# Kernel optimization log

Hardware: AMD Instinct MI355X
Metric: run time of the kernel (lower is better)

Reference implementation:

```python
import jax, jax.numpy as jnp
import numpy as np

N_NODES = 100000
N_EDGES = 1600000
D_IN = 64
D_H = 64
D_LIN = 256
D_OUT = 128
N_GRAPHS = 64
BN_EPS = 1e-5


def setup_inputs() -> dict:
    key = jax.random.key(0)
    ks = jax.random.split(key, 16)

    def lin(k, fan_in, fan_out):
        # kaiming-ish init, scale 1/sqrt(fan_in)
        return jax.random.normal(k, (fan_in, fan_out), jnp.float32) / np.float32(np.sqrt(fan_in))

    inp = {}
    inp["x"] = jax.random.normal(ks[0], (N_NODES, D_IN), jnp.float32)
    inp["edge_index"] = jax.random.randint(ks[1], (2, N_EDGES), 0, N_NODES, jnp.int32)
    inp["batch"] = jnp.sort(jax.random.randint(ks[2], (N_NODES,), 0, N_GRAPHS, jnp.int32))

    dims = [(D_IN, D_H), (D_H, D_H), (D_H, D_H)]
    ki = 3
    for l, (di, do) in enumerate(dims):
        inp[f"conv{l}_w1"] = lin(ks[ki], di, do); ki += 1
        inp[f"conv{l}_b1"] = jnp.zeros((do,), jnp.float32)
        inp[f"conv{l}_w2"] = lin(ks[ki], do, do); ki += 1
        inp[f"conv{l}_b2"] = jnp.zeros((do,), jnp.float32)
    for l in range(2):
        inp[f"bn{l}_gamma"] = jnp.ones((D_H,), jnp.float32)
        inp[f"bn{l}_beta"] = jnp.zeros((D_H,), jnp.float32)
    inp["mp_w1"] = lin(ks[ki], D_H, D_LIN); ki += 1
    inp["mp_b1"] = jnp.zeros((D_LIN,), jnp.float32)
    inp["mp_w2"] = lin(ks[ki], D_LIN, D_OUT)
    inp["mp_b2"] = jnp.zeros((D_OUT,), jnp.float32)
    return inp


def gin_conv(x, src, dst, w1, b1, w2, b2):
    # GINConv with eps=0: nn((1+eps)*x + sum_{j->i} x_j)
    agg = jax.ops.segment_sum(x[src], dst, num_segments=N_NODES)  # [N, d]
    h = x + agg
    h = jnp.maximum(h @ w1 + b1, 0.0)
    return h @ w2 + b2


def batch_norm(x, gamma, beta):
    # BatchNorm1d over node dim (training-mode batch statistics)
    mean = jnp.mean(x, axis=0)
    var = jnp.var(x, axis=0)
    return (x - mean) * jax.lax.rsqrt(var + BN_EPS) * gamma + beta


def reference(x, edge_index, batch,
              conv0_w1, conv0_b1, conv0_w2, conv0_b2,
              conv1_w1, conv1_b1, conv1_w2, conv1_b2,
              conv2_w1, conv2_b1, conv2_w2, conv2_b2,
              bn0_gamma, bn0_beta, bn1_gamma, bn1_beta,
              mp_w1, mp_b1, mp_w2, mp_b2):
    src, dst = edge_index[0], edge_index[1]
    convs = [(conv0_w1, conv0_b1, conv0_w2, conv0_b2),
             (conv1_w1, conv1_b1, conv1_w2, conv1_b2),
             (conv2_w1, conv2_b1, conv2_w2, conv2_b2)]
    bns = [(bn0_gamma, bn0_beta), (bn1_gamma, bn1_beta)]

    h = x
    # first conv_num_layers-1 layers: conv -> BN -> ReLU (dropout = identity in eval)
    for i in range(2):
        w1, b1, w2, b2 = convs[i]
        h = gin_conv(h, src, dst, w1, b1, w2, b2)
        h = batch_norm(h, bns[i][0], bns[i][1])
        h = jnp.maximum(h, 0.0)
    # last conv
    w1, b1, w2, b2 = convs[2]
    h = gin_conv(h, src, dst, w1, b1, w2, b2)
    # global add pool over graphs
    pooled = jax.ops.segment_sum(h, batch, num_segments=N_GRAPHS)  # [G, d]
    emb = pooled
    out = jnp.maximum(pooled @ mp_w1 + mp_b1, 0.0)  # dropout = identity in eval
    out = out @ mp_w2 + mp_b2
    return (out, emb)
```

## Files before the change

kernel.cpp:

```cpp
#include <hip/hip_runtime.h>

#define N_NODES 100000
#define N_EDGES 1600000
#define D 64
#define N_GRAPHS 64
#define D_LIN 256
#define D_OUT 128
#define BN_EPS 1e-5f
#define NBUCK 782
#define BIN_CH 16384
#define ESTAGE 1024

typedef unsigned short ushort;
typedef unsigned int uint;
typedef float floatx4 __attribute__((ext_vector_type(4)));
typedef uint uintx2 __attribute__((ext_vector_type(2)));

__device__ __forceinline__ float4 ld4(const float* p) { return *(const float4*)p; }

__device__ __forceinline__ uint f2bf(float f) {
  uint u = __float_as_uint(f);
  return (u + 0x7FFFu + ((u >> 16) & 1u)) >> 16;
}

__global__ __launch_bounds__(256) void k_cvt(const float* __restrict__ in,
                                             ushort* __restrict__ out, int n8) {
  int i = blockIdx.x * 256 + threadIdx.x;
  if (i < n8) {
    float4 a = ((const float4*)in)[2 * i];
    float4 b = ((const float4*)in)[2 * i + 1];
    uint4 o;
    o.x = f2bf(a.x) | (f2bf(a.y) << 16);
    o.y = f2bf(a.z) | (f2bf(a.w) << 16);
    o.z = f2bf(b.x) | (f2bf(b.y) << 16);
    o.w = f2bf(b.z) | (f2bf(b.w) << 16);
    ((uint4*)out)[i] = o;
  }
}

__global__ __launch_bounds__(256) void k_hist(const int* __restrict__ dstA,
                                              int* __restrict__ bcnt) {
  __shared__ int lh[NBUCK];
  for (int i = threadIdx.x; i < NBUCK; i += 256) lh[i] = 0;
  __syncthreads();
  int i = blockIdx.x * 256 + threadIdx.x;
  const int stride = gridDim.x * 256;
  for (; i < N_EDGES; i += stride) atomicAdd(&lh[dstA[i] >> 7], 1);
  __syncthreads();
  for (int i = threadIdx.x; i < NBUCK; i += 256)
    if (lh[i]) atomicAdd(&bcnt[i], lh[i]);
}

__global__ __launch_bounds__(1024) void k_bscan(const int* __restrict__ bcnt,
                                                int* __restrict__ boff,
                                                int* __restrict__ bcur) {
  __shared__ int s[1024];
  int t = threadIdx.x;
  int v = (t < NBUCK) ? bcnt[t] : 0;
  s[t] = v;
  __syncthreads();
  for (int off = 1; off < 1024; off <<= 1) {
    int u = (t >= off) ? s[t - off] : 0;
    __syncthreads();
    s[t] += u;
    __syncthreads();
  }
  if (t < NBUCK) {
    boff[t] = s[t] - v;
    bcur[t] = s[t] - v;
  }
}

__global__ __launch_bounds__(256) void k_bin(const int* __restrict__ srcA,
                                             const int* __restrict__ dstA,
                                             int* __restrict__ bcur,
                                             uint2* __restrict__ pairs) {
  __shared__ int lh[NBUCK];
  __shared__ int lbase[NBUCK];
  const int tid = threadIdx.x;
  for (int i = tid; i < NBUCK; i += 256) lh[i] = 0;
  __syncthreads();
  const int e0 = blockIdx.x * BIN_CH;
  const int e1 = min(e0 + BIN_CH, N_EDGES);
  for (int i = e0 + tid; i < e1; i += 256) atomicAdd(&lh[dstA[i] >> 7], 1);
  __syncthreads();
  for (int b = tid; b < NBUCK; b += 256) {
    int c = lh[b];
    if (c) lbase[b] = atomicAdd(&bcur[b], c);
  }
  __syncthreads();
  for (int b = tid; b < NBUCK; b += 256) lh[b] = 0;
  __syncthreads();
  for (int i = e0 + tid; i < e1; i += 256) {
    int d = dstA[i];
    int b = d >> 7;
    int p = lbase[b] + atomicAdd(&lh[b], 1);
    pairs[p] = make_uint2((uint)srcA[i], (uint)d);
  }
}

__global__ __launch_bounds__(256) void k_bucket(const uint2* __restrict__ pairs,
                                                const int* __restrict__ boff,
                                                const int* __restrict__ bcnt,
                                                int* __restrict__ rowptr,
                                                int* __restrict__ colidx) {
  __shared__ int ldeg[128], lsc[128], lcur[128];
  __shared__ int stage[4096];
  const int tid = threadIdx.x;
  const int b = blockIdx.x;
  const int node0 = b << 7;
  const int base = boff[b], cnt = bcnt[b];
  if (tid < 128) ldeg[tid] = 0;
  __syncthreads();
  for (int i = tid; i < cnt; i += 256) atomicAdd(&ldeg[pairs[base + i].y & 127], 1);
  __syncthreads();
  if (tid < 128) lsc[tid] = ldeg[tid];
  __syncthreads();
  for (int off = 1; off < 128; off <<= 1) {
    int u = (tid < 128 && tid >= off) ? lsc[tid - off] : 0;
    __syncthreads();
    if (tid < 128) lsc[tid] += u;
    __syncthreads();
  }
  if (tid < 128) {
    int excl = lsc[tid] - ldeg[tid];
    lcur[tid] = excl;
    int node = node0 + tid;
    if (node < N_NODES) rowptr[node] = base + excl;
  }
  if (b == NBUCK - 1 && tid == 0) rowptr[N_NODES] = N_EDGES;
  __syncthreads();
  if (cnt <= 4096) {
    for (int i = tid; i < cnt; i += 256) {
      uint2 pr = pairs[base + i];
      int p = atomicAdd(&lcur[pr.y & 127], 1);
      stage[p] = (int)pr.x;
    }
    __syncthreads();
    for (int i = tid; i < cnt; i += 256) colidx[base + i] = stage[i];
  } else {
    for (int i = tid; i < cnt; i += 256) {
      uint2 pr = pairs[base + i];
      int p = atomicAdd(&lcur[pr.y & 127], 1);
      colidx[base + p] = (int)pr.x;
    }
  }
}

template <int APPLY_BN, int EMIT_STATS, int OUT_BF>
__global__ __launch_bounds__(128, 6) void k_conv(
    const ushort* __restrict__ h_in, const float* __restrict__ ss,
    const int* __restrict__ rowptr, const int* __restrict__ colidx,
    const float* __restrict__ w1, const float* __restrict__ b1,
    const float* __restrict__ w2, const float* __restrict__ b2,
    float* __restrict__ h_out_f, ushort* __restrict__ h_out_bf,
    float* __restrict__ stats) {
  __shared__ float sT[32][68];
  __shared__ float sSum[64], sSq[64];
  __shared__ int sEdge[ESTAGE];
  __shared__ int sRp[33];

  const int tid = threadIdx.x;
  const int wave = tid >> 6, lane = tid & 63;
  const int g = lane >> 3;
  const int fl = (lane & 7) << 3;
  const int row0 = blockIdx.x * 32;

  if (EMIT_STATS && tid < 64) { sSum[tid] = 0.f; sSq[tid] = 0.f; }
  if (tid < 33) sRp[tid] = rowptr[row0 + tid];
  __syncthreads();

  const int ebase = sRp[0];
  const int ecnt = sRp[32] - ebase;
  const int estage = min(ecnt, ESTAGE);
  for (int i = tid; i < estage; i += 128)
    sEdge[i] = __builtin_nontemporal_load(colidx + ebase + i);
  __syncthreads();

  float sc[8], sh[8];
  if (APPLY_BN) {
    float4 a = ld4(&ss[fl]), b = ld4(&ss[fl + 4]);
    float4 c = ld4(&ss[64 + fl]), d = ld4(&ss[64 + fl + 4]);
    sc[0] = a.x; sc[1] = a.y; sc[2] = a.z; sc[3] = a.w;
    sc[4] = b.x; sc[5] = b.y; sc[6] = b.z; sc[7] = b.w;
    sh[0] = c.x; sh[1] = c.y; sh[2] = c.z; sh[3] = c.w;
    sh[4] = d.x; sh[5] = d.y; sh[6] = d.z; sh[7] = d.w;
  }

#define ACC8(u)                                                        \
  {                                                                    \
    float f0 = __uint_as_float((u).x << 16);                           \
    float f1 = __uint_as_float((u).x & 0xffff0000u);                   \
    float f2 = __uint_as_float((u).y << 16);                           \
    float f3 = __uint_as_float((u).y & 0xffff0000u);                   \
    float f4 = __uint_as_float((u).z << 16);                           \
    float f5 = __uint_as_float((u).z & 0xffff0000u);                   \
    float f6 = __uint_as_float((u).w << 16);                           \
    float f7 = __uint_as_float((u).w & 0xffff0000u);                   \
    if (APPLY_BN) {                                                    \
      f0 = fmaxf(fmaf(f0, sc[0], sh[0]), 0.f);                         \
      f1 = fmaxf(fmaf(f1, sc[1], sh[1]), 0.f);                         \
      f2 = fmaxf(fmaf(f2, sc[2], sh[2]), 0.f);                         \
      f3 = fmaxf(fmaf(f3, sc[3], sh[3]), 0.f);                         \
      f4 = fmaxf(fmaf(f4, sc[4], sh[4]), 0.f);                         \
      f5 = fmaxf(fmaf(f5, sc[5], sh[5]), 0.f);                         \
      f6 = fmaxf(fmaf(f6, sc[6], sh[6]), 0.f);                         \
      f7 = fmaxf(fmaf(f7, sc[7], sh[7]), 0.f);                         \
    }                                                                  \
    acc[0] += f0; acc[1] += f1; acc[2] += f2; acc[3] += f3;            \
    acc[4] += f4; acc[5] += f5; acc[6] += f6; acc[7] += f7;            \
  }
#define GATHER(s) *(const uint4*)(h_in + ((size_t)(s) << 6) + fl)

#pragma unroll
  for (int b = 0; b < 2; ++b) {
    const int r = (wave << 4) + (b << 3) + g;
    const int row = row0 + r;
    float acc[8] = {0.f, 0.f, 0.f, 0.f, 0.f, 0.f, 0.f, 0.f};
    {
      uint4 u = GATHER(row);
      ACC8(u);
    }
    const int re0 = sRp[r] - ebase;
    const int re1g = sRp[r + 1] - ebase;
    const int re1 = min(re1g, estage);
    int e = re0;
    for (; e + 7 < re1; e += 8) {
      int s0 = sEdge[e];
      int s1 = sEdge[e + 1];
      int s2 = sEdge[e + 2];
      int s3 = sEdge[e + 3];
      int s4 = sEdge[e + 4];
      int s5 = sEdge[e + 5];
      int s6 = sEdge[e + 6];
      int s7 = sEdge[e + 7];
      uint4 u0 = GATHER(s0);
      uint4 u1 = GATHER(s1);
      uint4 u2 = GATHER(s2);
      uint4 u3 = GATHER(s3);
      uint4 u4 = GATHER(s4);
      uint4 u5 = GATHER(s5);
      uint4 u6 = GATHER(s6);
      uint4 u7 = GATHER(s7);
      ACC8(u0); ACC8(u1); ACC8(u2); ACC8(u3);
      ACC8(u4); ACC8(u5); ACC8(u6); ACC8(u7);
    }
    if (e < re1) {
      const int em = re1 - 1;
      int s0 = sEdge[e];
      int s1 = sEdge[min(e + 1, em)];
      int s2 = sEdge[min(e + 2, em)];
      int s3 = sEdge[min(e + 3, em)];
      int s4 = sEdge[min(e + 4, em)];
      int s5 = sEdge[min(e + 5, em)];
      int s6 = sEdge[min(e + 6, em)];
      int s7 = sEdge[min(e + 7, em)];
      uint4 u0 = GATHER(s0);
      uint4 u1 = GATHER(s1);
      uint4 u2 = GATHER(s2);
      uint4 u3 = GATHER(s3);
      uint4 u4 = GATHER(s4);
      uint4 u5 = GATHER(s5);
      uint4 u6 = GATHER(s6);
      uint4 u7 = GATHER(s7);
      ACC8(u0);
      if (e + 1 < re1) ACC8(u1);
      if (e + 2 < re1) ACC8(u2);
      if (e + 3 < re1) ACC8(u3);
      if (e + 4 < re1) ACC8(u4);
      if (e + 5 < re1) ACC8(u5);
      if (e + 6 < re1) ACC8(u6);
      if (e + 7 < re1) ACC8(u7);
    }
    for (int eg2 = ebase + max(re0, estage); eg2 < ebase + re1g; ++eg2) {
      int s0 = colidx[eg2];
      uint4 u0 = GATHER(s0);
      ACC8(u0);
    }
    *(float4*)&sT[r][fl] = make_float4(acc[0], acc[1], acc[2], acc[3]);
    *(float4*)&sT[r][fl + 4] = make_float4(acc[4], acc[5], acc[6], acc[7]);
  }
#undef GATHER
#undef ACC8
  __syncthreads();

  const int tc = tid & 15, tr = tid >> 4;

  float hreg[4][4];
  {
    float acc[4][4];
#pragma unroll
    for (int i = 0; i < 4; ++i)
#pragma unroll
      for (int j = 0; j < 4; ++j) acc[i][j] = 0.f;
#pragma unroll 8
    for (int k = 0; k < 64; ++k) {
      const float4 b = ld4(&w1[(k << 6) + (tc << 2)]);
#pragma unroll
      for (int i = 0; i < 4; ++i) {
        const float a = sT[(tr << 2) + i][k];
        acc[i][0] = fmaf(a, b.x, acc[i][0]);
        acc[i][1] = fmaf(a, b.y, acc[i][1]);
        acc[i][2] = fmaf(a, b.z, acc[i][2]);
        acc[i][3] = fmaf(a, b.w, acc[i][3]);
      }
    }
    const float4 bb = ld4(&b1[tc << 2]);
#pragma unroll
    for (int i = 0; i < 4; ++i) {
      hreg[i][0] = fmaxf(acc[i][0] + bb.x, 0.f);
      hreg[i][1] = fmaxf(acc[i][1] + bb.y, 0.f);
      hreg[i][2] = fmaxf(acc[i][2] + bb.z, 0.f);
      hreg[i][3] = fmaxf(acc[i][3] + bb.w, 0.f);
    }
  }
  __syncthreads();
#pragma unroll
  for (int i = 0; i < 4; ++i)
    *(float4*)&sT[(tr << 2) + i][tc << 2] = *(float4*)&hreg[i][0];
  __syncthreads();

  {
    float acc[4][4];
#pragma unroll
    for (int i = 0; i < 4; ++i)
#pragma unroll
      for (int j = 0; j < 4; ++j) acc[i][j] = 0.f;
#pragma unroll 8
    for (int k = 0; k < 64; ++k) {
      const float4 b = ld4(&w2[(k << 6) + (tc << 2)]);
#pragma unroll
      for (int i = 0; i < 4; ++i) {
        const float a = sT[(tr << 2) + i][k];
        acc[i][0] = fmaf(a, b.x, acc[i][0]);
        acc[i][1] = fmaf(a, b.y, acc[i][1]);
        acc[i][2] = fmaf(a, b.z, acc[i][2]);
        acc[i][3] = fmaf(a, b.w, acc[i][3]);
      }
    }
    const float4 bb = ld4(&b2[tc << 2]);
    float p[4] = {0.f, 0.f, 0.f, 0.f}, q[4] = {0.f, 0.f, 0.f, 0.f};
#pragma unroll
    for (int i = 0; i < 4; ++i) {
      const int row = row0 + (tr << 2) + i;
      float4 o;
      o.x = acc[i][0] + bb.x;
      o.y = acc[i][1] + bb.y;
      o.z = acc[i][2] + bb.z;
      o.w = acc[i][3] + bb.w;
      if (OUT_BF) {
        uintx2 o2;
        o2.x = f2bf(o.x) | (f2bf(o.y) << 16);
        o2.y = f2bf(o.z) | (f2bf(o.w) << 16);
        __builtin_nontemporal_store(o2, (uintx2*)(h_out_bf + ((size_t)row << 6) + (tc << 2)));
      } else {
        floatx4 o4;
        o4.x = o.x; o4.y = o.y; o4.z = o.z; o4.w = o.w;
        __builtin_nontemporal_store(o4, (floatx4*)&h_out_f[row * 64 + (tc << 2)]);
      }
      if (EMIT_STATS) {
        p[0] += o.x; q[0] += o.x * o.x;
        p[1] += o.y; q[1] += o.y * o.y;
        p[2] += o.z; q[2] += o.z * o.z;
        p[3] += o.w; q[3] += o.w * o.w;
      }
    }
    if (EMIT_STATS) {
#pragma unroll
      for (int j = 0; j < 4; ++j) {
        atomicAdd(&sSum[(tc << 2) + j], p[j]);
        atomicAdd(&sSq[(tc << 2) + j], q[j]);
      }
      __syncthreads();
      if (tid < 64) {
        atomicAdd(&stats[tid], sSum[tid]);
        atomicAdd(&stats[64 + tid], sSq[tid]);
      }
    }
  }
}

__global__ void k_bnfin(const float* __restrict__ stats, const float* __restrict__ gamma,
                        const float* __restrict__ beta, float* __restrict__ ss) {
  int t = threadIdx.x;
  if (t < 64) {
    const float inv_n = 1.f / (float)N_NODES;
    float mean = stats[t] * inv_n;
    float var = stats[64 + t] * inv_n - mean * mean;
    float scale = gamma[t] * rsqrtf(var + BN_EPS);
    ss[t] = scale;
    ss[64 + t] = beta[t] - mean * scale;
  }
}

__global__ __launch_bounds__(256) void k_pool(const float* __restrict__ h,
                                              const int* __restrict__ batch,
                                              float* __restrict__ emb) {
  const int NW = 1024;
  const int RPW = (N_NODES + NW - 1) / NW;
  int wid = (blockIdx.x * 256 + threadIdx.x) >> 6;
  int lane = threadIdx.x & 63;
  int r0 = wid * RPW;
  if (r0 >= N_NODES) return;
  int r1 = min(r0 + RPW, N_NODES);
  float acc = 0.f;
  int curg = batch[r0];
  for (int i = r0; i < r1; ++i) {
    int g = batch[i];
    if (g != curg) {
      atomicAdd(&emb[curg * 64 + lane], acc);
      acc = 0.f;
      curg = g;
    }
    acc += h[i * 64 + lane];
  }
  atomicAdd(&emb[curg * 64 + lane], acc);
}

__global__ __launch_bounds__(256) void k_mlp(const float* __restrict__ emb,
                                             const float* __restrict__ w1,
                                             const float* __restrict__ b1,
                                             const float* __restrict__ w2,
                                             const float* __restrict__ b2,
                                             float* __restrict__ out) {
  __shared__ float sp[64];
  __shared__ float smid[256];
  int g = blockIdx.x, t = threadIdx.x;
  if (t < 64) sp[t] = emb[g * 64 + t];
  __syncthreads();
  float acc = b1[t];
#pragma unroll 8
  for (int k = 0; k < 64; ++k) acc = fmaf(sp[k], w1[k * 256 + t], acc);
  smid[t] = fmaxf(acc, 0.f);
  __syncthreads();
  if (t < 128) {
    float o = b2[t];
#pragma unroll 8
    for (int k = 0; k < 256; ++k) o = fmaf(smid[k], w2[k * 128 + t], o);
    out[g * 128 + t] = o;
  }
}

extern "C" void kernel_launch(void* const* d_in, const int* in_sizes, int n_in,
                              void* d_out, int out_size, void* d_ws, size_t ws_size,
                              hipStream_t stream) {
  const float* x = (const float*)d_in[0];
  const int* edge = (const int*)d_in[1];
  const int* batch = (const int*)d_in[2];
  const float* cw1[3] = {(const float*)d_in[3], (const float*)d_in[7], (const float*)d_in[11]};
  const float* cb1[3] = {(const float*)d_in[4], (const float*)d_in[8], (const float*)d_in[12]};
  const float* cw2[3] = {(const float*)d_in[5], (const float*)d_in[9], (const float*)d_in[13]};
  const float* cb2[3] = {(const float*)d_in[6], (const float*)d_in[10], (const float*)d_in[14]};
  const float* bng[2] = {(const float*)d_in[15], (const float*)d_in[17]};
  const float* bnb[2] = {(const float*)d_in[16], (const float*)d_in[18]};
  const float* mpw1 = (const float*)d_in[19];
  const float* mpb1 = (const float*)d_in[20];
  const float* mpw2 = (const float*)d_in[21];
  const float* mpb2 = (const float*)d_in[22];

  char* ws = (char*)d_ws;
  size_t off = 0;
  auto alloc = [&](size_t bytes) {
    void* p = ws + off;
    off = (off + bytes + 255) & ~(size_t)255;
    return p;
  };
  int* rowptr = (int*)alloc((N_NODES + 1) * sizeof(int));
  int* colidx = (int*)alloc(N_EDGES * sizeof(int));
  int* bcnt = (int*)alloc(NBUCK * sizeof(int));
  int* boff = (int*)alloc(NBUCK * sizeof(int));
  int* bcur = (int*)alloc(NBUCK * sizeof(int));
  ushort* x_bf = (ushort*)alloc((size_t)N_NODES * 64 * sizeof(ushort));
  ushort* hA_bf = (ushort*)alloc((size_t)N_NODES * 64 * sizeof(ushort));
  ushort* hB_bf = (ushort*)alloc((size_t)N_NODES * 64 * sizeof(ushort));
  float* stats = (float*)alloc(2 * 128 * sizeof(float));
  float* ssbuf = (float*)alloc(2 * 128 * sizeof(float));
  float* hF = (float*)x_bf;
  uint2* pairs = (uint2*)hB_bf;

  float* outp = (float*)d_out;
  float* emb = outp + N_GRAPHS * D_OUT;

  const int* srcA = edge;
  const int* dstA = edge + N_EDGES;

  hipMemsetAsync(bcnt, 0, NBUCK * sizeof(int), stream);
  hipMemsetAsync(stats, 0, 2 * 128 * sizeof(float), stream);
  hipMemsetAsync(emb, 0, N_GRAPHS * 64 * sizeof(float), stream);

  k_cvt<<<(N_NODES * 64 / 8 + 255) / 256, 256, 0, stream>>>(x, x_bf, N_NODES * 64 / 8);
  k_hist<<<256, 256, 0, stream>>>(dstA, bcnt);
  k_bscan<<<1, 1024, 0, stream>>>(bcnt, boff, bcur);
  k_bin<<<(N_EDGES + BIN_CH - 1) / BIN_CH, 256, 0, stream>>>(srcA, dstA, bcur, pairs);
  k_bucket<<<NBUCK, 256, 0, stream>>>(pairs, boff, bcnt, rowptr, colidx);

  const int GC = N_NODES / 32;
  k_conv<0, 1, 1><<<GC, 128, 0, stream>>>(x_bf, nullptr, rowptr, colidx, cw1[0], cb1[0],
                                          cw2[0], cb2[0], nullptr, hA_bf, stats);
  k_bnfin<<<1, 64, 0, stream>>>(stats, bng[0], bnb[0], ssbuf);
  k_conv<1, 1, 1><<<GC, 128, 0, stream>>>(hA_bf, ssbuf, rowptr, colidx, cw1[1], cb1[1],
                                          cw2[1], cb2[1], nullptr, hB_bf, stats + 128);
  k_bnfin<<<1, 64, 0, stream>>>(stats + 128, bng[1], bnb[1], ssbuf + 128);
  k_conv<1, 0, 0><<<GC, 128, 0, stream>>>(hB_bf, ssbuf + 128, rowptr, colidx, cw1[2],
                                          cb1[2], cw2[2], cb2[2], hF, nullptr, nullptr);

  k_pool<<<256, 256, 0, stream>>>(hF, batch, emb);
  k_mlp<<<N_GRAPHS, 256, 0, stream>>>(emb, mpw1, mpb1, mpw2, mpb2, outp);
}
```

Baseline: 473.3 us.

## Shrink conv blocks to one wave, degree-sort rows, unroll gathers by 16

```diff
diff --git a/kernel.cpp b/kernel.cpp
--- a/kernel.cpp
+++ b/kernel.cpp
@@ -9,7 +9,7 @@
 #define BN_EPS 1e-5f
 #define NBUCK 782
 #define BIN_CH 16384
-#define ESTAGE 1024
+#define ESTAGE 768
 
 typedef unsigned short ushort;
 typedef unsigned int uint;
@@ -148,32 +148,44 @@
 }
 
 template <int APPLY_BN, int EMIT_STATS, int OUT_BF>
-__global__ __launch_bounds__(128, 6) void k_conv(
+__global__ __launch_bounds__(64, 4) void k_conv(
     const ushort* __restrict__ h_in, const float* __restrict__ ss,
     const int* __restrict__ rowptr, const int* __restrict__ colidx,
     const float* __restrict__ w1, const float* __restrict__ b1,
     const float* __restrict__ w2, const float* __restrict__ b2,
     float* __restrict__ h_out_f, ushort* __restrict__ h_out_bf,
     float* __restrict__ stats) {
-  __shared__ float sT[32][68];
+  __shared__ float sT[16][68];
   __shared__ float sSum[64], sSq[64];
   __shared__ int sEdge[ESTAGE];
-  __shared__ int sRp[33];
+  __shared__ int sRp[17];
+  __shared__ int sDeg[16], sOrd[16];
 
   const int tid = threadIdx.x;
-  const int wave = tid >> 6, lane = tid & 63;
-  const int g = lane >> 3;
-  const int fl = (lane & 7) << 3;
-  const int row0 = blockIdx.x * 32;
-
-  if (EMIT_STATS && tid < 64) { sSum[tid] = 0.f; sSq[tid] = 0.f; }
-  if (tid < 33) sRp[tid] = rowptr[row0 + tid];
-  __syncthreads();
+  const int g = tid >> 3;
+  const int fl = (tid & 7) << 3;
+  const int row0 = blockIdx.x * 16;
+
+  if (EMIT_STATS) { sSum[tid] = 0.f; sSq[tid] = 0.f; }
+  if (tid < 17) sRp[tid] = rowptr[row0 + tid];
+  __syncthreads();
+  if (tid < 16) sDeg[tid] = sRp[tid + 1] - sRp[tid];
+  __syncthreads();
+  if (tid < 16) {
+    const int d = sDeg[tid];
+    int rk = 0;
+#pragma unroll
+    for (int j = 0; j < 16; ++j) {
+      int dj = sDeg[j];
+      rk += (dj < d) || (dj == d && j < tid);
+    }
+    sOrd[rk] = tid;
+  }
 
   const int ebase = sRp[0];
-  const int ecnt = sRp[32] - ebase;
+  const int ecnt = sRp[16] - ebase;
   const int estage = min(ecnt, ESTAGE);
-  for (int i = tid; i < estage; i += 128)
+  for (int i = tid; i < estage; i += 64)
     sEdge[i] = __builtin_nontemporal_load(colidx + ebase + i);
   __syncthreads();
 
@@ -214,7 +226,7 @@
 
 #pragma unroll
   for (int b = 0; b < 2; ++b) {
-    const int r = (wave << 4) + (b << 3) + g;
+    const int r = sOrd[(b << 3) + g];
     const int row = row0 + r;
     float acc[8] = {0.f, 0.f, 0.f, 0.f, 0.f, 0.f, 0.f, 0.f};
     {
@@ -225,52 +237,28 @@
     const int re1g = sRp[r + 1] - ebase;
     const int re1 = min(re1g, estage);
     int e = re0;
-    for (; e + 7 < re1; e += 8) {
-      int s0 = sEdge[e];
-      int s1 = sEdge[e + 1];
-      int s2 = sEdge[e + 2];
-      int s3 = sEdge[e + 3];
-      int s4 = sEdge[e + 4];
-      int s5 = sEdge[e + 5];
-      int s6 = sEdge[e + 6];
-      int s7 = sEdge[e + 7];
-      uint4 u0 = GATHER(s0);
-      uint4 u1 = GATHER(s1);
-      uint4 u2 = GATHER(s2);
-      uint4 u3 = GATHER(s3);
-      uint4 u4 = GATHER(s4);
-      uint4 u5 = GATHER(s5);
-      uint4 u6 = GATHER(s6);
-      uint4 u7 = GATHER(s7);
-      ACC8(u0); ACC8(u1); ACC8(u2); ACC8(u3);
-      ACC8(u4); ACC8(u5); ACC8(u6); ACC8(u7);
+    for (; e + 15 < re1; e += 16) {
+      int s[16];
+#pragma unroll
+      for (int j = 0; j < 16; ++j) s[j] = sEdge[e + j];
+      uint4 u[16];
+#pragma unroll
+      for (int j = 0; j < 16; ++j) u[j] = GATHER(s[j]);
+#pragma unroll
+      for (int j = 0; j < 16; ++j) ACC8(u[j]);
     }
     if (e < re1) {
       const int em = re1 - 1;
-      int s0 = sEdge[e];
-      int s1 = sEdge[min(e + 1, em)];
-      int s2 = sEdge[min(e + 2, em)];
-      int s3 = sEdge[min(e + 3, em)];
-      int s4 = sEdge[min(e + 4, em)];
-      int s5 = sEdge[min(e + 5, em)];
-      int s6 = sEdge[min(e + 6, em)];
-      int s7 = sEdge[min(e + 7, em)];
-      uint4 u0 = GATHER(s0);
-      uint4 u1 = GATHER(s1);
-      uint4 u2 = GATHER(s2);
-      uint4 u3 = GATHER(s3);
-      uint4 u4 = GATHER(s4);
-      uint4 u5 = GATHER(s5);
-      uint4 u6 = GATHER(s6);
-      uint4 u7 = GATHER(s7);
-      ACC8(u0);
-      if (e + 1 < re1) ACC8(u1);
-      if (e + 2 < re1) ACC8(u2);
-      if (e + 3 < re1) ACC8(u3);
-      if (e + 4 < re1) ACC8(u4);
-      if (e + 5 < re1) ACC8(u5);
-      if (e + 6 < re1) ACC8(u6);
-      if (e + 7 < re1) ACC8(u7);
+      int s[16];
+#pragma unroll
+      for (int j = 0; j < 16; ++j) s[j] = sEdge[min(e + j, em)];
+      uint4 u[16];
+#pragma unroll
+      for (int j = 0; j < 16; ++j) u[j] = GATHER(s[j]);
+      ACC8(u[0]);
+#pragma unroll
+      for (int j = 1; j < 16; ++j)
+        if (e + j < re1) ACC8(u[j]);
     }
     for (int eg2 = ebase + max(re0, estage); eg2 < ebase + re1g; ++eg2) {
       int s0 = colidx[eg2];
@@ -372,10 +360,8 @@
         atomicAdd(&sSq[(tc << 2) + j], q[j]);
       }
       __syncthreads();
-      if (tid < 64) {
-        atomicAdd(&stats[tid], sSum[tid]);
-        atomicAdd(&stats[64 + tid], sSq[tid]);
-      }
+      atomicAdd(&stats[tid], sSum[tid]);
+      atomicAdd(&stats[64 + tid], sSq[tid]);
     }
   }
 }
@@ -494,15 +480,15 @@
   k_bin<<<(N_EDGES + BIN_CH - 1) / BIN_CH, 256, 0, stream>>>(srcA, dstA, bcur, pairs);
   k_bucket<<<NBUCK, 256, 0, stream>>>(pairs, boff, bcnt, rowptr, colidx);
 
-  const int GC = N_NODES / 32;
-  k_conv<0, 1, 1><<<GC, 128, 0, stream>>>(x_bf, nullptr, rowptr, colidx, cw1[0], cb1[0],
-                                          cw2[0], cb2[0], nullptr, hA_bf, stats);
+  const int GC = N_NODES / 16;
+  k_conv<0, 1, 1><<<GC, 64, 0, stream>>>(x_bf, nullptr, rowptr, colidx, cw1[0], cb1[0],
+                                         cw2[0], cb2[0], nullptr, hA_bf, stats);
   k_bnfin<<<1, 64, 0, stream>>>(stats, bng[0], bnb[0], ssbuf);
-  k_conv<1, 1, 1><<<GC, 128, 0, stream>>>(hA_bf, ssbuf, rowptr, colidx, cw1[1], cb1[1],
-                                          cw2[1], cb2[1], nullptr, hB_bf, stats + 128);
+  k_conv<1, 1, 1><<<GC, 64, 0, stream>>>(hA_bf, ssbuf, rowptr, colidx, cw1[1], cb1[1],
+                                         cw2[1], cb2[1], nullptr, hB_bf, stats + 128);
   k_bnfin<<<1, 64, 0, stream>>>(stats + 128, bng[1], bnb[1], ssbuf + 128);
-  k_conv<1, 0, 0><<<GC, 128, 0, stream>>>(hB_bf, ssbuf + 128, rowptr, colidx, cw1[2],
-                                          cb1[2], cw2[2], cb2[2], hF, nullptr, nullptr);
+  k_conv<1, 0, 0><<<GC, 64, 0, stream>>>(hB_bf, ssbuf + 128, rowptr, colidx, cw1[2],
+                                         cb1[2], cw2[2], cb2[2], hF, nullptr, nullptr);
 
   k_pool<<<256, 256, 0, stream>>>(hF, batch, emb);
   k_mlp<<<N_GRAPHS, 256, 0, stream>>>(emb, mpw1, mpb1, mpw2, mpb2, outp);
```

After: 600.3 us. +26.8%, slower.
